# Kernel optimization log

Measured on AMD Instinct MI355X. Metric: run time of the kernel, lower is better.

## Reference

```python
import jax, jax.numpy as jnp
import numpy as np

N = 100000
E = 1600000
D = 128      # input_dim == hidden_dim
L = 3        # num_layers
EPS = 1e-5


def setup_inputs() -> dict:
    key = jax.random.key(0)
    ks = jax.random.split(key, 12)
    s = 1.0 / np.sqrt(D)
    return {
        "x": jax.random.normal(ks[0], (N, D), jnp.float32),
        "edge_index": jax.random.randint(ks[1], (2, E), 0, N, jnp.int32),
        "reranker_scores": jax.random.normal(ks[2], (N,), jnp.float32),
        # input residual projection
        "proj_w": jax.random.normal(ks[3], (D, D), jnp.float32) * s,
        "proj_b": jnp.zeros((D,), jnp.float32),
        # SAGEConv weights (lin_l: aggregated neighbors, with bias; lin_r: root, no bias)
        "lin_l_w": jax.random.normal(ks[4], (L, D, D), jnp.float32) * s,
        "lin_l_b": jnp.zeros((L, D), jnp.float32),
        "lin_r_w": jax.random.normal(ks[5], (L, D, D), jnp.float32) * s,
        # layer norm params
        "ln_g": jnp.ones((L, D), jnp.float32),
        "ln_b": jnp.zeros((L, D), jnp.float32),
        # score head
        "head_w": jax.random.normal(ks[6], (D,), jnp.float32) * s,
        "head_b": jnp.zeros((), jnp.float32),
        "alpha": jnp.asarray(0.65, jnp.float32),
    }


def _layer_norm(h, g, b):
    mu = jnp.mean(h, axis=-1, keepdims=True)
    var = jnp.mean(jnp.square(h - mu), axis=-1, keepdims=True)
    return (h - mu) * jax.lax.rsqrt(var + EPS) * g + b


def reference(x, edge_index, reranker_scores, proj_w, proj_b,
              lin_l_w, lin_l_b, lin_r_w, ln_g, ln_b, head_w, head_b, alpha):
    src, dst = edge_index[0], edge_index[1]
    # in-degree for mean aggregation (clamped to avoid div-by-zero)
    deg = jax.ops.segment_sum(jnp.ones((E,), x.dtype), dst, num_segments=N)
    inv_deg = (1.0 / jnp.maximum(deg, 1.0))[:, None]  # [N,1]

    residual = x @ proj_w.T + proj_b  # input_proj(x)
    h = x
    for i in range(L):
        # SAGEConv(mean): lin_l(mean_{j->i} h_j) + lin_r(h_i)
        agg = jax.ops.segment_sum(h[src], dst, num_segments=N) * inv_deg
        h_new = agg @ lin_l_w[i].T + lin_l_b[i] + h @ lin_r_w[i].T
        h_new = jax.nn.relu(h_new)
        h_new = _layer_norm(h_new, ln_g[i], ln_b[i])
        # dropout p=0.0 -> identity
        h_new = h_new + (residual if i == 0 else h)
        h = h_new
    gnn_scores = h @ head_w + head_b  # [N]
    a = jax.nn.sigmoid(alpha)
    return a * reranker_scores + (1.0 - a) * gnn_scores
```

## Files before the change

kernel.cpp:

```cpp
#include <hip/hip_runtime.h>
#include <math.h>

#define N_NODES 100000
#define N_EDGES 1600000
#define D 128
#define NBKT 391

#define PREP_WL 48
#define PREP_WR 48
#define PREP_PJ 16
#define PREP_X  12500
#define PREP_BC 391

typedef __attribute__((ext_vector_type(8))) short short8;
typedef __attribute__((ext_vector_type(4))) float floatx4;

__device__ __forceinline__ float bf2f(unsigned short u) {
    union { unsigned int i; float f; } v;
    v.i = ((unsigned int)u) << 16;
    return v.f;
}
__device__ __forceinline__ unsigned short f2bf(float f) {
    union { float f; unsigned int i; } v;
    v.f = f;
    unsigned int u = v.i;
    u += 0x7fffu + ((u >> 16) & 1u);
    return (unsigned short)(u >> 16);
}
__device__ __forceinline__ unsigned short f2h(float f) {
    union { _Float16 h; unsigned short u; } c;
    c.h = (_Float16)f;
    return c.u;
}
__device__ __forceinline__ float h2f(unsigned short u) {
    union { unsigned short u; _Float16 h; } c;
    c.u = u;
    return (float)c.h;
}

__device__ __forceinline__ void split8(const float* __restrict__ p, short8& hi, short8& lo) {
    float4 v0 = *(const float4*)p;
    float4 v1 = *(const float4*)(p + 4);
    float f[8] = {v0.x, v0.y, v0.z, v0.w, v1.x, v1.y, v1.z, v1.w};
#pragma unroll
    for (int i = 0; i < 8; ++i) {
        unsigned short h = f2bf(f[i]);
        hi[i] = (short)h;
        lo[i] = (short)f2bf(f[i] - bf2f(h));
    }
}

typedef __attribute__((address_space(3))) unsigned short lds_us;
typedef __attribute__((address_space(1))) const unsigned short gl_us;

__device__ __forceinline__ void stageG(unsigned short* sWbuf,
                                       const unsigned short* __restrict__ W, int tid) {
#pragma unroll
    for (int i = 0; i < 4; ++i) {
        int e = tid + 512 * i;
        int ct = e >> 8;
        int ks = (e >> 6) & 3;
        int q = (e >> 4) & 3;
        int l = e & 15;
        const unsigned short* g = W + (size_t)(ct * 16 + l) * D + ks * 32 + q * 8;
        unsigned short* lp = sWbuf + (size_t)(i * 512 + (tid & ~63)) * 8;
        __builtin_amdgcn_global_load_lds((gl_us*)g, (lds_us*)lp, 16, 0, 0);
    }
}

template <bool DUAL>
__device__ __forceinline__ void computeP(const unsigned short* sWbuf, int lane,
                                         const short8* Ah, const short8* Al, floatx4* acc) {
#pragma unroll
    for (int ks = 0; ks < 4; ++ks)
#pragma unroll
        for (int ct = 0; ct < 8; ++ct) {
            short8 wf = *(const short8*)(sWbuf + ((ct * 4 + ks) * 64 + lane) * 8);
            acc[ct] = __builtin_amdgcn_mfma_f32_16x16x32_bf16(Ah[ks], wf, acc[ct], 0, 0, 0);
            if (DUAL)
                acc[ct] = __builtin_amdgcn_mfma_f32_16x16x32_bf16(Al[ks], wf, acc[ct], 0, 0, 0);
        }
}

__device__ __forceinline__ void cvt_split_body(const float* __restrict__ s,
                                               unsigned short* __restrict__ hi,
                                               unsigned short* __restrict__ lo,
                                               int lb, int n4, int tid) {
    int i = lb * 256 + tid;
    if (i < n4) {
        float4 v = ((const float4*)s)[i];
        float f[4] = {v.x, v.y, v.z, v.w};
        ushort4 h, l;
        unsigned short* hp = (unsigned short*)&h;
        unsigned short* lp = (unsigned short*)&l;
#pragma unroll
        for (int c = 0; c < 4; ++c) {
            unsigned short hh = f2bf(f[c]);
            hp[c] = hh;
            lp[c] = f2bf(f[c] - bf2f(hh));
        }
        ((ushort4*)hi)[i] = h;
        ((ushort4*)lo)[i] = l;
    }
}

__global__ __launch_bounds__(256) void k_prep(
    const float* __restrict__ WlAll, unsigned short* __restrict__ Wlh, unsigned short* __restrict__ Wll,
    const float* __restrict__ WrAll, unsigned short* __restrict__ Wrh, unsigned short* __restrict__ Wrl,
    const float* __restrict__ projW, unsigned short* __restrict__ pWh, unsigned short* __restrict__ pWl,
    const float* __restrict__ x, unsigned short* __restrict__ xf,
    const int* __restrict__ dst, int* __restrict__ bcnt) {
    __shared__ int h[NBKT];
    int tid = threadIdx.x;
    int b = blockIdx.x;
    if (b < PREP_WL) { cvt_split_body(WlAll, Wlh, Wll, b, 3 * D * D / 4, tid); return; }
    b -= PREP_WL;
    if (b < PREP_WR) { cvt_split_body(WrAll, Wrh, Wrl, b, 3 * D * D / 4, tid); return; }
    b -= PREP_WR;
    if (b < PREP_PJ) { cvt_split_body(projW, pWh, pWl, b, D * D / 4, tid); return; }
    b -= PREP_PJ;
    if (b < PREP_X) {
        int i = b * 256 + tid;
        if (i < N_NODES * D / 4) {
            float4 v = ((const float4*)x)[i];
            ushort4 o;
            o.x = f2h(v.x); o.y = f2h(v.y); o.z = f2h(v.z); o.w = f2h(v.w);
            ((ushort4*)xf)[i] = o;
        }
        return;
    }
    b -= PREP_X;
    for (int i = tid; i < NBKT; i += 256) h[i] = 0;
    __syncthreads();
    int e0 = b * 4096;
#pragma unroll
    for (int i = 0; i < 16; ++i) {
        int e = e0 + tid + i * 256;
        if (e < N_EDGES) atomicAdd(&h[dst[e] >> 8], 1);
    }
    __syncthreads();
    for (int i = tid; i < NBKT; i += 256) {
        int c = h[i];
        if (c) atomicAdd(&bcnt[i], c);
    }
}

__global__ void k_bscan(const int* __restrict__ bcnt, int* __restrict__ bbase,
                        int* __restrict__ bcur, int* __restrict__ offs) {
    __shared__ int tmp[512];
    int tid = threadIdx.x;
    int v = (tid < NBKT) ? bcnt[tid] : 0;
    tmp[tid] = v;
    __syncthreads();
    for (int off = 1; off < 512; off <<= 1) {
        int t = (tid >= off) ? tmp[tid - off] : 0;
        __syncthreads();
        if (tid >= off) tmp[tid] += t;
        __syncthreads();
    }
    int ex = tmp[tid] - v;
    if (tid < NBKT) {
        bbase[tid] = ex;
        bcur[tid] = ex;
    }
    if (tid == 0) {
        bbase[NBKT] = N_EDGES;
        offs[N_NODES] = N_EDGES;
    }
}

__global__ __launch_bounds__(256) void k_bucket(const int* __restrict__ src,
                                                const int* __restrict__ dst,
                                                int* __restrict__ bcur, uint2* __restrict__ pairs) {
    __shared__ int cnt[NBKT];
    __shared__ int off[NBKT];
    int tid = threadIdx.x;
    for (int i = tid; i < NBKT; i += 256) cnt[i] = 0;
    __syncthreads();
    int e0 = blockIdx.x * 4096;
    int mydst[16], mysrc[16];
#pragma unroll
    for (int i = 0; i < 16; ++i) {
        int e = e0 + tid + i * 256;
        int d = (e < N_EDGES) ? dst[e] : -1;
        mydst[i] = d;
        mysrc[i] = (e < N_EDGES) ? src[e] : 0;
        if (d >= 0) atomicAdd(&cnt[d >> 8], 1);
    }
    __syncthreads();
    for (int b = tid; b < NBKT; b += 256) {
        int c = cnt[b];
        off[b] = c ? atomicAdd(&bcur[b], c) : 0;
    }
    __syncthreads();
#pragma unroll
    for (int i = 0; i < 16; ++i) {
        int d = mydst[i];
        if (d >= 0) {
            int p = atomicAdd(&off[d >> 8], 1);
            pairs[p] = make_uint2((unsigned)mysrc[i], (unsigned)d);
        }
    }
}

__global__ __launch_bounds__(256) void k_build(const uint2* __restrict__ pairs,
                                               const int* __restrict__ bbase,
                                               int* __restrict__ offs, float* __restrict__ invd,
                                               int* __restrict__ csr_src) {
    __shared__ int cnt[256];
    __shared__ int scn[256];
    __shared__ int cur[256];
    int b = blockIdx.x, tid = threadIdx.x;
    int node0 = b << 8;
    int nn = N_NODES - node0; if (nn > 256) nn = 256;
    int beg = bbase[b], end = bbase[b + 1];

    cnt[tid] = 0;
    __syncthreads();
    for (int e = beg + tid; e < end; e += 256) atomicAdd(&cnt[pairs[e].y & 255u], 1);
    __syncthreads();
    int v = cnt[tid];
    scn[tid] = v;
    __syncthreads();
    for (int off = 1; off < 256; off <<= 1) {
        int t = (tid >= off) ? scn[tid - off] : 0;
        __syncthreads();
        if (tid >= off) scn[tid] += t;
        __syncthreads();
    }
    int start = beg + scn[tid] - v;
    if (tid < nn) {
        offs[node0 + tid] = start;
        invd[node0 + tid] = 1.0f / (float)(v > 1 ? v : 1);
    }
    cur[tid] = start;
    __syncthreads();
    for (int e = beg + tid; e < end; e += 256) {
        uint2 pr = pairs[e];
        int p = atomicAdd(&cur[pr.y & 255u], 1);
        csr_src[p] = (int)pr.x;
    }
}

__global__ void k_agg_f16(const unsigned short* __restrict__ hf, const int* __restrict__ offs,
                          const int* __restrict__ csr_src, const float* __restrict__ inv_deg,
                          float* __restrict__ agg) {
    int gw = (blockIdx.x * 256 + threadIdx.x) >> 6;
    int lane = threadIdx.x & 63;
    int half = lane >> 5, l32 = lane & 31;
    int node = gw * 2 + half;
    int beg = offs[node], end = offs[node + 1];
    float a0 = 0.f, a1 = 0.f, a2 = 0.f, a3 = 0.f;
    int e = beg;
    for (; e + 7 < end; e += 8) {
        int ss[8];
#pragma unroll
        for (int i = 0; i < 8; ++i) ss[i] = csr_src[e + i];
        uint2 vv[8];
#pragma unroll
        for (int i = 0; i < 8; ++i)
            vv[i] = ((const uint2*)(hf + (size_t)ss[i] * D))[l32];
#pragma unroll
        for (int i = 0; i < 8; ++i) {
            a0 += h2f((unsigned short)(vv[i].x & 0xffffu));
            a1 += h2f((unsigned short)(vv[i].x >> 16));
            a2 += h2f((unsigned short)(vv[i].y & 0xffffu));
            a3 += h2f((unsigned short)(vv[i].y >> 16));
        }
    }
    for (; e + 3 < end; e += 4) {
        int ss[4];
#pragma unroll
        for (int i = 0; i < 4; ++i) ss[i] = csr_src[e + i];
        uint2 vv[4];
#pragma unroll
        for (int i = 0; i < 4; ++i)
            vv[i] = ((const uint2*)(hf + (size_t)ss[i] * D))[l32];
#pragma unroll
        for (int i = 0; i < 4; ++i) {
            a0 += h2f((unsigned short)(vv[i].x & 0xffffu));
            a1 += h2f((unsigned short)(vv[i].x >> 16));
            a2 += h2f((unsigned short)(vv[i].y & 0xffffu));
            a3 += h2f((unsigned short)(vv[i].y >> 16));
        }
    }
    for (; e < end; ++e) {
        int s = csr_src[e];
        uint2 v = ((const uint2*)(hf + (size_t)s * D))[l32];
        a0 += h2f((unsigned short)(v.x & 0xffffu));
        a1 += h2f((unsigned short)(v.x >> 16));
        a2 += h2f((unsigned short)(v.y & 0xffffu));
        a3 += h2f((unsigned short)(v.y >> 16));
    }
    float id = inv_deg[node];
    float4 o;
    o.x = a0 * id; o.y = a1 * id; o.z = a2 * id; o.w = a3 * id;
    ((float4*)(agg + (size_t)node * D))[l32] = o;
}

template <int MODE>
__global__ __launch_bounds__(512) void k_layer(
    const float* __restrict__ aggf, const float* __restrict__ hinf,
    const float* __restrict__ skipf,
    const unsigned short* __restrict__ Wlh, const unsigned short* __restrict__ Wll,
    const unsigned short* __restrict__ Wrh, const unsigned short* __restrict__ Wrl,
    const unsigned short* __restrict__ pWh, const unsigned short* __restrict__ pWl,
    const float* __restrict__ projB,
    const float* __restrict__ lb, const float* __restrict__ g,
    const float* __restrict__ beta,
    float* __restrict__ hout, unsigned short* __restrict__ houtf,
    const float* __restrict__ hw, const float* __restrict__ hb_bias,
    const float* __restrict__ rr, const float* __restrict__ alphap,
    float* __restrict__ outp) {
    __shared__ unsigned short sW[2][16384];

    int tid = threadIdx.x;
    int w = tid >> 6, lane = tid & 63;
    int quad = lane >> 4, l16 = lane & 15;
    int base = blockIdx.x * 128 + w * 16;

    int ar = base + l16; if (ar > N_NODES - 1) ar = N_NODES - 1;
    const float* aggr = aggf + (size_t)ar * D;
    const float* hinr = hinf + (size_t)ar * D;
    int koff = quad * 8;

    floatx4 z = {0.f, 0.f, 0.f, 0.f};
    floatx4 acc[8];
#pragma unroll
    for (int ct = 0; ct < 8; ++ct) acc[ct] = z;

    stageG(sW[0], Wlh, tid);
    short8 ah[4], al[4];
#pragma unroll
    for (int ks = 0; ks < 4; ++ks) split8(aggr + ks * 32 + koff, ah[ks], al[ks]);
    __syncthreads();

    stageG(sW[1], Wll, tid);
    computeP<true>(sW[0], lane, ah, al, acc);
    __syncthreads();

    stageG(sW[0], Wrh, tid);
    short8 bh[4], blo[4];
#pragma unroll
    for (int ks = 0; ks < 4; ++ks) split8(hinr + ks * 32 + koff, bh[ks], blo[ks]);
    computeP<false>(sW[1], lane, ah, al, acc);
    __syncthreads();

    stageG(sW[1], Wrl, tid);
    computeP<true>(sW[0], lane, bh, blo, acc);
    __syncthreads();

    if (MODE == 0) stageG(sW[0], pWh, tid);
    computeP<false>(sW[1], lane, bh, blo, acc);

    floatx4 accR[8];
    if (MODE == 0) {
#pragma unroll
        for (int ct = 0; ct < 8; ++ct) accR[ct] = z;
        __syncthreads();
        stageG(sW[1], pWl, tid);
        computeP<true>(sW[0], lane, bh, blo, accR);
        __syncthreads();
        computeP<false>(sW[1], lane, bh, blo, accR);
    }

    float lbv[8], gv[8], bv[8];
#pragma unroll
    for (int ct = 0; ct < 8; ++ct) {
        int n = ct * 16 + l16;
        lbv[ct] = lb[n];
        gv[ct] = g[n];
        bv[ct] = beta[n];
    }
#pragma unroll
    for (int ct = 0; ct < 8; ++ct)
#pragma unroll
        for (int r = 0; r < 4; ++r)
            acc[ct][r] = fmaxf(acc[ct][r] + lbv[ct], 0.f);

    float mu[4], rs[4];
#pragma unroll
    for (int r = 0; r < 4; ++r) {
        float s = 0.f, ss = 0.f;
#pragma unroll
        for (int ct = 0; ct < 8; ++ct) {
            float v = acc[ct][r];
            s += v;
            ss += v * v;
        }
#pragma unroll
        for (int m = 1; m < 16; m <<= 1) {
            s += __shfl_xor(s, m, 64);
            ss += __shfl_xor(ss, m, 64);
        }
        float m_ = s * (1.0f / 128.0f);
        float v_ = ss * (1.0f / 128.0f) - m_ * m_;
        mu[r] = m_;
        rs[r] = rsqrtf(v_ + 1e-5f);
    }

    float pbv[8], hwv[8];
    if (MODE == 0) {
#pragma unroll
        for (int ct = 0; ct < 8; ++ct) pbv[ct] = projB[ct * 16 + l16];
    }
    if (MODE == 2) {
#pragma unroll
        for (int ct = 0; ct < 8; ++ct) hwv[ct] = hw[ct * 16 + l16];
    }

#pragma unroll
    for (int r = 0; r < 4; ++r) {
        int crow = base + quad * 4 + r;
        bool valid = (crow < N_NODES);
        float m_ = mu[r], rs_ = rs[r];
        size_t ro = (size_t)crow * D;
        if (MODE == 2) {
            float s = 0.f;
#pragma unroll
            for (int ct = 0; ct < 8; ++ct) {
                int col = ct * 16 + l16;
                float sk = valid ? skipf[ro + col] : 0.f;
                float o = (acc[ct][r] - m_) * rs_ * gv[ct] + bv[ct] + sk;
                s += o * hwv[ct];
            }
#pragma unroll
            for (int m = 1; m < 16; m <<= 1) s += __shfl_xor(s, m, 64);
            if (l16 == 0 && valid) {
                float a = 1.0f / (1.0f + expf(-alphap[0]));
                outp[crow] = a * rr[crow] + (1.0f - a) * (s + hb_bias[0]);
            }
        } else {
            if (!valid) continue;
#pragma unroll
            for (int ct = 0; ct < 8; ++ct) {
                int col = ct * 16 + l16;
                float sk = (MODE == 0) ? (accR[ct][r] + pbv[ct]) : skipf[ro + col];
                float o = (acc[ct][r] - m_) * rs_ * gv[ct] + bv[ct] + sk;
                hout[ro + col] = o;
                houtf[ro + col] = f2h(o);
            }
        }
    }
}

extern "C" void kernel_launch(void* const* d_in, const int* in_sizes, int n_in,
                              void* d_out, int out_size, void* d_ws, size_t ws_size,
                              hipStream_t stream) {
    const float* x     = (const float*)d_in[0];
    const int*   ei    = (const int*)d_in[1];
    const float* rr    = (const float*)d_in[2];
    const float* projW = (const float*)d_in[3];
    const float* projB = (const float*)d_in[4];
    const float* WlAll = (const float*)d_in[5];
    const float* lbAll = (const float*)d_in[6];
    const float* WrAll = (const float*)d_in[7];
    const float* gAll  = (const float*)d_in[8];
    const float* btAll = (const float*)d_in[9];
    const float* hw    = (const float*)d_in[10];
    const float* hbias = (const float*)d_in[11];
    const float* alpha = (const float*)d_in[12];
    float* out = (float*)d_out;

    char* p = (char*)d_ws;
    float* agg = (float*)p; p += (size_t)N_NODES * D * 4;
    float* h0  = (float*)p; p += (size_t)N_NODES * D * 4;
    float* h1  = (float*)p; p += (size_t)N_NODES * D * 4;
    unsigned short* h0f = (unsigned short*)p; p += (size_t)N_NODES * D * 2;
    unsigned short* h1f = (unsigned short*)p; p += (size_t)N_NODES * D * 2;
    unsigned short* Wlh = (unsigned short*)p; p += (size_t)3 * D * D * 2;
    unsigned short* Wll = (unsigned short*)p; p += (size_t)3 * D * D * 2;
    unsigned short* Wrh = (unsigned short*)p; p += (size_t)3 * D * D * 2;
    unsigned short* Wrl = (unsigned short*)p; p += (size_t)3 * D * D * 2;
    unsigned short* pWh = (unsigned short*)p; p += (size_t)D * D * 2;
    unsigned short* pWl = (unsigned short*)p; p += (size_t)D * D * 2;
    float* invd  = (float*)p; p += (size_t)N_NODES * 4;
    int* offs    = (int*)p; p += (size_t)(N_NODES + 2) * 4;
    int* csr_src = (int*)p; p += (size_t)N_EDGES * 4;
    int* bcnt    = (int*)p; p += 512 * 4;
    int* bbase   = (int*)p; p += 512 * 4;
    int* bcur    = (int*)p; p += 512 * 4;

    unsigned short* xf = (unsigned short*)h1;
    uint2* pairs = (uint2*)h0;

    const int* src = ei;
    const int* dst = ei + N_EDGES;

    hipMemsetAsync(bcnt, 0, 512 * 4, stream);
    k_prep<<<PREP_WL + PREP_WR + PREP_PJ + PREP_X + PREP_BC, 256, 0, stream>>>(
        WlAll, Wlh, Wll, WrAll, Wrh, Wrl, projW, pWh, pWl, x, xf, dst, bcnt);
    k_bscan<<<1, 512, 0, stream>>>(bcnt, bbase, bcur, offs);
    k_bucket<<<NBKT, 256, 0, stream>>>(src, dst, bcur, pairs);
    k_build<<<NBKT, 256, 0, stream>>>(pairs, bbase, offs, invd, csr_src);

    int gl = (N_NODES + 127) / 128;
    int ga = N_NODES / 2 / 4;

    k_agg_f16<<<ga, 256, 0, stream>>>(xf, offs, csr_src, invd, agg);
    k_layer<0><<<gl, 512, 0, stream>>>(agg, x, nullptr,
                                       Wlh, Wll, Wrh, Wrl, pWh, pWl, projB,
                                       lbAll, gAll, btAll, h0, h0f,
                                       nullptr, nullptr, nullptr, nullptr, nullptr);
    k_agg_f16<<<ga, 256, 0, stream>>>(h0f, offs, csr_src, invd, agg);
    k_layer<1><<<gl, 512, 0, stream>>>(agg, h0, h0,
                                       Wlh + D * D, Wll + D * D, Wrh + D * D, Wrl + D * D,
                                       nullptr, nullptr, nullptr,
                                       lbAll + D, gAll + D, btAll + D, h1, h1f,
                                       nullptr, nullptr, nullptr, nullptr, nullptr);
    k_agg_f16<<<ga, 256, 0, stream>>>(h1f, offs, csr_src, invd, agg);
    k_layer<2><<<gl, 512, 0, stream>>>(agg, h1, h1,
                                       Wlh + 2 * D * D, Wll + 2 * D * D,
                                       Wrh + 2 * D * D, Wrl + 2 * D * D,
                                       nullptr, nullptr, nullptr,
                                       lbAll + 2 * D, gAll + 2 * D, btAll + 2 * D,
                                       nullptr, nullptr,
                                       hw, hbias, rr, alpha, out);
}
```

Before: 530.7 us.

## Fuse neighbor mean aggregation into the layer GEMM kernel

```diff
diff --git a/kernel.cpp b/kernel.cpp
--- a/kernel.cpp
+++ b/kernel.cpp
@@ -48,6 +48,17 @@
         hi[i] = (short)h;
         lo[i] = (short)f2bf(f[i] - bf2f(h));
     }
+}
+
+__device__ __forceinline__ void acc8(float* s, uint4 v) {
+    s[0] += h2f((unsigned short)(v.x & 0xffffu));
+    s[1] += h2f((unsigned short)(v.x >> 16));
+    s[2] += h2f((unsigned short)(v.y & 0xffffu));
+    s[3] += h2f((unsigned short)(v.y >> 16));
+    s[4] += h2f((unsigned short)(v.z & 0xffffu));
+    s[5] += h2f((unsigned short)(v.z >> 16));
+    s[6] += h2f((unsigned short)(v.w & 0xffffu));
+    s[7] += h2f((unsigned short)(v.w >> 16));
 }
 
 typedef __attribute__((address_space(3))) unsigned short lds_us;
@@ -242,66 +253,12 @@
     }
 }
 
-__global__ void k_agg_f16(const unsigned short* __restrict__ hf, const int* __restrict__ offs,
-                          const int* __restrict__ csr_src, const float* __restrict__ inv_deg,
-                          float* __restrict__ agg) {
-    int gw = (blockIdx.x * 256 + threadIdx.x) >> 6;
-    int lane = threadIdx.x & 63;
-    int half = lane >> 5, l32 = lane & 31;
-    int node = gw * 2 + half;
-    int beg = offs[node], end = offs[node + 1];
-    float a0 = 0.f, a1 = 0.f, a2 = 0.f, a3 = 0.f;
-    int e = beg;
-    for (; e + 7 < end; e += 8) {
-        int ss[8];
-#pragma unroll
-        for (int i = 0; i < 8; ++i) ss[i] = csr_src[e + i];
-        uint2 vv[8];
-#pragma unroll
-        for (int i = 0; i < 8; ++i)
-            vv[i] = ((const uint2*)(hf + (size_t)ss[i] * D))[l32];
-#pragma unroll
-        for (int i = 0; i < 8; ++i) {
-            a0 += h2f((unsigned short)(vv[i].x & 0xffffu));
-            a1 += h2f((unsigned short)(vv[i].x >> 16));
-            a2 += h2f((unsigned short)(vv[i].y & 0xffffu));
-            a3 += h2f((unsigned short)(vv[i].y >> 16));
-        }
-    }
-    for (; e + 3 < end; e += 4) {
-        int ss[4];
-#pragma unroll
-        for (int i = 0; i < 4; ++i) ss[i] = csr_src[e + i];
-        uint2 vv[4];
-#pragma unroll
-        for (int i = 0; i < 4; ++i)
-            vv[i] = ((const uint2*)(hf + (size_t)ss[i] * D))[l32];
-#pragma unroll
-        for (int i = 0; i < 4; ++i) {
-            a0 += h2f((unsigned short)(vv[i].x & 0xffffu));
-            a1 += h2f((unsigned short)(vv[i].x >> 16));
-            a2 += h2f((unsigned short)(vv[i].y & 0xffffu));
-            a3 += h2f((unsigned short)(vv[i].y >> 16));
-        }
-    }
-    for (; e < end; ++e) {
-        int s = csr_src[e];
-        uint2 v = ((const uint2*)(hf + (size_t)s * D))[l32];
-        a0 += h2f((unsigned short)(v.x & 0xffffu));
-        a1 += h2f((unsigned short)(v.x >> 16));
-        a2 += h2f((unsigned short)(v.y & 0xffffu));
-        a3 += h2f((unsigned short)(v.y >> 16));
-    }
-    float id = inv_deg[node];
-    float4 o;
-    o.x = a0 * id; o.y = a1 * id; o.z = a2 * id; o.w = a3 * id;
-    ((float4*)(agg + (size_t)node * D))[l32] = o;
-}
-
 template <int MODE>
 __global__ __launch_bounds__(512) void k_layer(
-    const float* __restrict__ aggf, const float* __restrict__ hinf,
-    const float* __restrict__ skipf,
+    const unsigned short* __restrict__ hf,
+    const int* __restrict__ offs, const int* __restrict__ csr_src,
+    const float* __restrict__ invd,
+    const float* __restrict__ hinf, const float* __restrict__ skipf,
     const unsigned short* __restrict__ Wlh, const unsigned short* __restrict__ Wll,
     const unsigned short* __restrict__ Wrh, const unsigned short* __restrict__ Wrl,
     const unsigned short* __restrict__ pWh, const unsigned short* __restrict__ pWl,
@@ -320,22 +277,63 @@
     int base = blockIdx.x * 128 + w * 16;
 
     int ar = base + l16; if (ar > N_NODES - 1) ar = N_NODES - 1;
-    const float* aggr = aggf + (size_t)ar * D;
     const float* hinr = hinf + (size_t)ar * D;
     int koff = quad * 8;
 
+    stageG(sW[0], Wlh, tid);
+    stageG(sW[1], Wll, tid);
+
+    int beg = offs[ar], end = offs[ar + 1];
+    float id = invd[ar];
+    float sm[4][8];
+#pragma unroll
+    for (int ks = 0; ks < 4; ++ks)
+#pragma unroll
+        for (int c = 0; c < 8; ++c) sm[ks][c] = 0.f;
+
+    int e = beg;
+    for (; e + 1 < end; e += 2) {
+        int n0 = csr_src[e], n1 = csr_src[e + 1];
+        uint4 v0[4], v1[4];
+#pragma unroll
+        for (int ks = 0; ks < 4; ++ks)
+            v0[ks] = *(const uint4*)(hf + (size_t)n0 * D + ks * 32 + koff);
+#pragma unroll
+        for (int ks = 0; ks < 4; ++ks)
+            v1[ks] = *(const uint4*)(hf + (size_t)n1 * D + ks * 32 + koff);
+#pragma unroll
+        for (int ks = 0; ks < 4; ++ks) acc8(sm[ks], v0[ks]);
+#pragma unroll
+        for (int ks = 0; ks < 4; ++ks) acc8(sm[ks], v1[ks]);
+    }
+    if (e < end) {
+        int n0 = csr_src[e];
+        uint4 v0[4];
+#pragma unroll
+        for (int ks = 0; ks < 4; ++ks)
+            v0[ks] = *(const uint4*)(hf + (size_t)n0 * D + ks * 32 + koff);
+#pragma unroll
+        for (int ks = 0; ks < 4; ++ks) acc8(sm[ks], v0[ks]);
+    }
+
+    short8 ah[4], al[4];
+#pragma unroll
+    for (int ks = 0; ks < 4; ++ks)
+#pragma unroll
+        for (int c = 0; c < 8; ++c) {
+            float f = sm[ks][c] * id;
+            unsigned short hh = f2bf(f);
+            ah[ks][c] = (short)hh;
+            al[ks][c] = (short)f2bf(f - bf2f(hh));
+        }
+
     floatx4 z = {0.f, 0.f, 0.f, 0.f};
     floatx4 acc[8];
 #pragma unroll
     for (int ct = 0; ct < 8; ++ct) acc[ct] = z;
 
-    stageG(sW[0], Wlh, tid);
-    short8 ah[4], al[4];
-#pragma unroll
-    for (int ks = 0; ks < 4; ++ks) split8(aggr + ks * 32 + koff, ah[ks], al[ks]);
-    __syncthreads();
-
-    stageG(sW[1], Wll, tid);
+    __syncthreads();
+
     computeP<true>(sW[0], lane, ah, al, acc);
     __syncthreads();
 
@@ -480,6 +478,7 @@
     int* bcnt    = (int*)p; p += 512 * 4;
     int* bbase   = (int*)p; p += 512 * 4;
     int* bcur    = (int*)p; p += 512 * 4;
+    (void)agg;
 
     unsigned short* xf = (unsigned short*)h1;
     uint2* pairs = (uint2*)h0;
@@ -495,21 +494,17 @@
     k_build<<<NBKT, 256, 0, stream>>>(pairs, bbase, offs, invd, csr_src);
 
     int gl = (N_NODES + 127) / 128;
-    int ga = N_NODES / 2 / 4;
-
-    k_agg_f16<<<ga, 256, 0, stream>>>(xf, offs, csr_src, invd, agg);
-    k_layer<0><<<gl, 512, 0, stream>>>(agg, x, nullptr,
+
+    k_layer<0><<<gl, 512, 0, stream>>>(xf, offs, csr_src, invd, x, nullptr,
                                        Wlh, Wll, Wrh, Wrl, pWh, pWl, projB,
                                        lbAll, gAll, btAll, h0, h0f,
                                        nullptr, nullptr, nullptr, nullptr, nullptr);
-    k_agg_f16<<<ga, 256, 0, stream>>>(h0f, offs, csr_src, invd, agg);
-    k_layer<1><<<gl, 512, 0, stream>>>(agg, h0, h0,
+    k_layer<1><<<gl, 512, 0, stream>>>(h0f, offs, csr_src, invd, h0, h0,
                                        Wlh + D * D, Wll + D * D, Wrh + D * D, Wrl + D * D,
                                        nullptr, nullptr, nullptr,
                                        lbAll + D, gAll + D, btAll + D, h1, h1f,
                                        nullptr, nullptr, nullptr, nullptr, nullptr);
-    k_agg_f16<<<ga, 256, 0, stream>>>(h1f, offs, csr_src, invd, agg);
-    k_layer<2><<<gl, 512, 0, stream>>>(agg, h1, h1,
+    k_layer<2><<<gl, 512, 0, stream>>>(h1f, offs, csr_src, invd, h1, h1,
                                        Wlh + 2 * D * D, Wll + 2 * D * D,
                                        Wrh + 2 * D * D, Wrl + 2 * D * D,
                                        nullptr, nullptr, nullptr,
```

Result: slower. 581.1 us (+9.5%).
